# Kernel tuning notes

Measured on AMD Instinct MI355X. Metric: run time of the kernel, lower is better.

Reference implementation:

```python
import jax, jax.numpy as jnp
import numpy as np

# ---- fan-beam CT geometry (hard-coded in fidelity_module) ----
N = 256                      # image is N x N on [-20, 20]^2
A = 20                       # number of projection angles over [0, 2pi)
UDET = 624                   # detector pixels on [-60, 60]
S = 768                      # ray samples for line-integral quadrature
R_SRC = 59.0                 # source-to-origin radius
R_DET = 49.0                 # detector-to-origin radius
D_SD = R_SRC + R_DET         # source-to-detector distance
XMIN, XMAX = -20.0, 20.0
DX = (XMAX - XMIN) / N
UMIN, UMAX = -60.0, 60.0
DU = (UMAX - UMIN) / UDET
THETAS = ((np.arange(A) + 0.5) * 2.0 * np.pi / A).astype(np.float32)   # cell midpoints (odl.uniform_partition)
UCENT = (UMIN + (np.arange(UDET) + 0.5) * DU).astype(np.float32)       # detector cell midpoints
NFFT = 2048                  # FFT length for ramp filtering (>= 2*UDET)


def _bilinear(img, gx, gy):
    """img: [B,N,N] (axis0=x, axis1=y). gx, gy: fractional index coords, shape [...].
    Returns [B, ...] with zero outside the image."""
    i0 = jnp.floor(gx)
    j0 = jnp.floor(gy)
    fx = (gx - i0).astype(img.dtype)
    fy = (gy - j0).astype(img.dtype)
    i0 = i0.astype(jnp.int32)
    j0 = j0.astype(jnp.int32)

    def corner(ii, jj):
        valid = (ii >= 0) & (ii < N) & (jj >= 0) & (jj < N)
        v = img[:, jnp.clip(ii, 0, N - 1), jnp.clip(jj, 0, N - 1)]
        return jnp.where(valid[None], v, 0.0)

    return (corner(i0, j0) * (1 - fx) * (1 - fy)
            + corner(i0 + 1, j0) * fx * (1 - fy)
            + corner(i0, j0 + 1) * (1 - fx) * fy
            + corner(i0 + 1, j0 + 1) * fx * fy)


def forward_project(img):
    """Ray-driven fan-beam forward projection (Radon transform). img: [B,N,N] -> sino [B,A,UDET]."""
    cs = jnp.cos(jnp.asarray(THETAS))
    sn = jnp.sin(jnp.asarray(THETAS))
    src = R_SRC * jnp.stack([cs, sn], axis=-1)            # (A,2) source positions
    det_c = -R_DET * jnp.stack([cs, sn], axis=-1)         # (A,2) detector centers
    ddir = jnp.stack([-sn, cs], axis=-1)                  # (A,2) detector axis
    u = jnp.asarray(UCENT)
    p = det_c[:, None, :] + u[None, :, None] * ddir[:, None, :]   # (A,U,2) detector pixel positions
    ray = p - src[:, None, :]                             # (A,U,2)
    length = jnp.sqrt(jnp.sum(ray * ray, axis=-1))        # (A,U) ray length
    tt = (jnp.arange(S, dtype=jnp.float32) + 0.5) / S     # (S,) midpoint quadrature
    pts = src[:, None, None, :] + tt[None, None, :, None] * ray[:, :, None, :]  # (A,U,S,2)
    gx = (pts[..., 0] - XMIN) / DX - 0.5                  # fractional index along axis0 (x)
    gy = (pts[..., 1] - XMIN) / DX - 0.5                  # fractional index along axis1 (y)
    vals = _bilinear(img, gx, gy)                         # (B,A,U,S)
    return jnp.sum(vals, axis=-1) * (length / S)[None]    # (B,A,U)


def fbp(sino):
    """Filtered back-projection with Hann-windowed ramp filter (frequency_scaling=1).
    sino: [B,A,UDET] -> image [B,N,N]."""
    u = jnp.asarray(UCENT)
    # cosine pre-weighting for flat fan-beam detector
    g = sino * (D_SD / jnp.sqrt(D_SD * D_SD + u * u))[None, None, :]
    freqs = jnp.fft.rfftfreq(NFFT, d=DU).astype(jnp.float32)
    nyq = 1.0 / (2.0 * DU)
    ramp = jnp.abs(freqs)
    hann = 0.5 * (1.0 + jnp.cos(np.float32(np.pi) * freqs / nyq)) * (freqs <= nyq)
    filt = ramp * hann
    q = jnp.fft.irfft(jnp.fft.rfft(g, n=NFFT, axis=-1) * filt[None, None, :], n=NFFT, axis=-1)
    q = q[..., :UDET] * DU                                # (B,A,U) filtered sinogram

    cs = jnp.cos(jnp.asarray(THETAS))
    sn = jnp.sin(jnp.asarray(THETAS))
    xs = XMIN + (jnp.arange(N, dtype=jnp.float32) + 0.5) * DX
    X = xs[:, None]                                       # axis0 = x
    Y = xs[None, :]                                       # axis1 = y
    # distance from source plane to pixel along central ray: in [R_SRC-28, R_SRC+28], never ~0
    tdist = R_SRC - (X[None] * cs[:, None, None] + Y[None] * sn[:, None, None])   # (A,N,N)
    uu = D_SD * (-X[None] * sn[:, None, None] + Y[None] * cs[:, None, None]) / tdist  # detector coord of pixel
    k = (uu - UCENT[0]) / DU                              # fractional detector index (A,N,N)
    k0 = jnp.floor(k)
    fk = (k - k0).astype(sino.dtype)
    k0 = k0.astype(jnp.int32)
    aidx = jnp.arange(A)[:, None, None]

    def gather(kk):
        valid = (kk >= 0) & (kk < UDET)
        v = q[:, aidx, jnp.clip(kk, 0, UDET - 1)]         # (B,A,N,N)
        return jnp.where(valid[None], v, 0.0)

    val = gather(k0) * (1 - fk)[None] + gather(k0 + 1) * fk[None]
    w = (R_SRC / tdist) ** 2                              # fan-beam distance weighting
    dtheta = 2.0 * np.pi / A
    return 0.5 * np.float32(dtheta) * jnp.sum(w[None] * val, axis=1)  # (B,N,N)


def setup_inputs() -> dict:
    key = jax.random.key(0)
    k1, k2 = jax.random.split(key)
    input_data = jax.random.uniform(k1, (4, N, N), dtype=jnp.float32)
    proj = jax.random.normal(k2, (4, A, UDET), dtype=jnp.float32)
    return {"input_data": input_data, "proj": proj}


def reference(input_data, proj):
    # fidelity_module.forward: x_error = FBP(proj - Radon(input_data))
    p_tmp = forward_project(input_data)
    y_error = proj - p_tmp
    return fbp(y_error)
```

## Files before the change

kernel.cpp:

```cpp
#include <hip/hip_runtime.h>
#include <math.h>

#define NN 256
#define AA 20
#define UD 624
#define SS 768
#define NAU (AA*UD)
#define PI_D 3.14159265358979323846

__global__ __launch_bounds__(256) void k_prep(const float* __restrict__ img,
                                              float4* __restrict__ pixA,
                                              float4* __restrict__ pixB,
                                              float* __restrict__ hh) {
    __shared__ double red[256];
    const int blk = blockIdx.x;
    const int tid = threadIdx.x;
    if (blk < 256) {
        int idx = blk * 256 + tid;
        float4 v;
        v.x = img[idx]; v.y = img[65536 + idx]; v.z = img[131072 + idx]; v.w = img[196608 + idx];
        pixA[idx] = v;
    } else if (blk < 512) {
        int oidx = (blk - 256) * 256 + tid;
        int j = oidx >> 8, i = oidx & 255;
        int idx = i * 256 + j;
        float4 v;
        v.x = img[idx]; v.y = img[65536 + idx]; v.z = img[131072 + idx]; v.w = img[196608 + idx];
        pixB[oidx] = v;
    } else {
        const int n = blk - 512;
        double acc = 0.0;
        for (int k = 1 + tid; k < 1024; k += 256) {
            float a1 = 1.0f + cosf((float)PI_D * (float)k * (1.0f/1024.0f));
            int m = (k * n) & 2047;
            float c2 = cosf((float)PI_D * (float)m * (1.0f/1024.0f));
            acc += (double)((float)k * a1 * c2);
        }
        red[tid] = acc;
        __syncthreads();
        for (int s = 128; s > 0; s >>= 1) {
            if (tid < s) red[tid] += red[tid + s];
            __syncthreads();
        }
        if (tid == 0) hh[n] = (float)(red[0] * (1.0 / (2048.0 * 2048.0)));
    }
}

__global__ __launch_bounds__(256) void k_fwd(const float4* __restrict__ pixA,
                                             const float4* __restrict__ pixB,
                                             const float* __restrict__ proj,
                                             float* __restrict__ g) {
    const int widx = threadIdx.x >> 6;
    const int lane = threadIdx.x & 63;
    const int qd = blockIdx.x * 4 + widx;
    const int a = qd / 156;
    const int ub = (qd - a * 156) * 4;
    const int grp = lane >> 4;
    const int sl = lane & 15;

    const float theta = (float)(((double)a + 0.5) * (2.0 * PI_D / (double)AA));
    float sn, cs;
    sincosf(theta, &sn, &cs);
    const float uc = (float)(-60.0 + ((double)(ub + grp) + 0.5) * (120.0 / 624.0));

    const float sx = 59.0f * cs, sy = 59.0f * sn;
    const float rx = -108.0f * cs - uc * sn;
    const float ry = -108.0f * sn + uc * cs;
    const float length = sqrtf(rx * rx + ry * ry);

    const float stepx = rx * (6.4f / 768.0f);
    const float basex = (sx + rx * (0.5f / 768.0f) + 20.0f) * 6.4f - 0.5f;
    const float stepy = ry * (6.4f / 768.0f);
    const float basey = (sy + ry * (0.5f / 768.0f) + 20.0f) * 6.4f - 0.5f;

    const bool useB = fabsf(stepx) > fabsf(stepy);
    const float4* __restrict__ im = useB ? pixB : pixA;
    const float bi = useB ? basex : basey;
    const float si = useB ? stepx : stepy;
    const float bo = useB ? basey : basex;
    const float so = useB ? stepy : stepx;

    float ax = 0.f, ay = 0.f, az = 0.f, aw = 0.f;

    for (int it = 0; it < 48; ++it) {
        const int s = (it << 4) + sl;
        float gi = fmaf((float)s, si, bi);
        float go = fmaf((float)s, so, bo);
        float fgi = floorf(gi), fgo = floorf(go);
        float fi = gi - fgi, fo = go - fgo;
        int i0 = (int)fgi, o0 = (int)fgo;
        int i1 = i0 + 1, o1 = o0 + 1;
        float wi0 = (i0 >= 0 && i0 < NN) ? (1.0f - fi) : 0.0f;
        float wi1 = (i1 >= 0 && i1 < NN) ? fi : 0.0f;
        float wo0 = (o0 >= 0 && o0 < NN) ? (1.0f - fo) : 0.0f;
        float wo1 = (o1 >= 0 && o1 < NN) ? fo : 0.0f;
        int ic0 = min(max(i0, 0), NN - 1), ic1 = min(max(i1, 0), NN - 1);
        int oc0 = min(max(o0, 0), NN - 1), oc1 = min(max(o1, 0), NN - 1);
        const float4 c00 = im[oc0 * NN + ic0];
        const float4 c10 = im[oc0 * NN + ic1];
        const float4 c01 = im[oc1 * NN + ic0];
        const float4 c11 = im[oc1 * NN + ic1];
        float w00 = wi0 * wo0, w10 = wi1 * wo0, w01 = wi0 * wo1, w11 = wi1 * wo1;
        ax += w00 * c00.x + w10 * c10.x + w01 * c01.x + w11 * c11.x;
        ay += w00 * c00.y + w10 * c10.y + w01 * c01.y + w11 * c11.y;
        az += w00 * c00.z + w10 * c10.z + w01 * c01.z + w11 * c11.z;
        aw += w00 * c00.w + w10 * c10.w + w01 * c01.w + w11 * c11.w;
    }

    for (int off = 8; off > 0; off >>= 1) {
        ax += __shfl_down(ax, off);
        ay += __shfl_down(ay, off);
        az += __shfl_down(az, off);
        aw += __shfl_down(aw, off);
    }

    if (sl == 0) {
        const int ray = a * UD + ub + grp;
        const float scale = length * (1.0f / 768.0f);
        const float wdet = 108.0f / sqrtf(108.0f * 108.0f + uc * uc);
        g[0 * NAU + ray] = (proj[0 * NAU + ray] - ax * scale) * wdet;
        g[1 * NAU + ray] = (proj[1 * NAU + ray] - ay * scale) * wdet;
        g[2 * NAU + ray] = (proj[2 * NAU + ray] - az * scale) * wdet;
        g[3 * NAU + ray] = (proj[3 * NAU + ray] - aw * scale) * wdet;
    }
}

__global__ __launch_bounds__(256) void k_conv(const float* __restrict__ g,
                                              const float* __restrict__ hh,
                                              float* __restrict__ q) {
    __shared__ float sgp[752];
    __shared__ float sacc[256];
    const int row = blockIdx.x / 10;
    const int jt = blockIdx.x - row * 10;
    const int tid = threadIdx.x;

    for (int k = tid; k < 752; k += 256)
        sgp[k] = (k >= 64 && k < 64 + UD) ? g[row * UD + (k - 64)] : 0.0f;
    __syncthreads();

    const int jloc = tid & 63;
    const int seg = tid >> 6;
    const int j = jt * 64 + jloc;
    const int jc = min(j, UD - 1);
    const int n1 = min(jt * 64 + 64, UD);
    const int n2 = UD - 1 - jt * 64;

    float acc = 0.0f;
    int t0 = (n1 * seg) >> 2, t1 = (n1 * (seg + 1)) >> 2;
    for (int t = t0; t < t1; ++t) acc += hh[t] * sgp[64 + jc - t];
    t0 = 1 + ((n2 * seg) >> 2); t1 = 1 + ((n2 * (seg + 1)) >> 2);
    for (int t = t0; t < t1; ++t) acc += hh[t] * sgp[64 + jc + t];

    sacc[tid] = acc;
    __syncthreads();
    if (tid < 64) {
        int jj = jt * 64 + tid;
        if (jj < UD) {
            float s = sacc[tid] + sacc[64 + tid] + sacc[128 + tid] + sacc[192 + tid];
            q[row * UD + jj] = s;
        }
    }
}

__global__ __launch_bounds__(256) void k_bp(const float* __restrict__ q,
                                            float* __restrict__ out) {
    __shared__ float scs[AA], ssn[AA];
    const int tid = threadIdx.x;
    if (tid < AA) {
        float th = (float)(((double)tid + 0.5) * (2.0 * PI_D / (double)AA));
        float s, c;
        sincosf(th, &s, &c);
        scs[tid] = c;
        ssn[tid] = s;
    }
    __syncthreads();

    const int p = blockIdx.x * 256 + tid;
    const int b = p >> 16;
    const int rem = p & 65535;
    const int i = rem >> 8;
    const int j = rem & 255;

    const float X = -20.0f + ((float)i + 0.5f) * 0.15625f;
    const float Y = -20.0f + ((float)j + 0.5f) * 0.15625f;

    const float uc0 = (float)(-60.0 + 0.5 * (120.0 / 624.0));
    const float duf = (float)(120.0 / 624.0);

    const float* __restrict__ qb = q + b * AA * UD;
    float acc = 0.0f;
#pragma unroll
    for (int a = 0; a < AA; ++a) {
        float cs = scs[a], sn = ssn[a];
        float t = 59.0f - (X * cs + Y * sn);
        float uu = 108.0f * (Y * cs - X * sn) / t;
        float k = (uu - uc0) / duf;
        float fk0 = floorf(k);
        float fk = k - fk0;
        int ik = (int)fk0;
        const float* qr = qb + a * UD;
        float v0 = ((unsigned)ik < (unsigned)UD) ? qr[ik] : 0.0f;
        float v1 = ((unsigned)(ik + 1) < (unsigned)UD) ? qr[ik + 1] : 0.0f;
        float val = v0 * (1.0f - fk) + v1 * fk;
        float w = 59.0f / t;
        acc += w * w * val;
    }
    out[p] = (0.5f * (float)(2.0 * PI_D / (double)AA)) * acc;
}

extern "C" void kernel_launch(void* const* d_in, const int* in_sizes, int n_in,
                              void* d_out, int out_size, void* d_ws, size_t ws_size,
                              hipStream_t stream) {
    const float* img  = (const float*)d_in[0];
    const float* proj = (const float*)d_in[1];
    float* out = (float*)d_out;

    char* ws = (char*)d_ws;
    float4* pixA = (float4*)ws;
    float4* pixB = (float4*)(ws + (1 << 20));
    float*  g    = (float*)(ws + (2 << 20));
    float*  q    = (float*)(ws + (2 << 20) + 200704);
    float*  hh   = (float*)(ws + (2 << 20) + 401408);

    k_prep<<<1136, 256, 0, stream>>>(img, pixA, pixB, hh);
    k_fwd <<<780,  256, 0, stream>>>(pixA, pixB, proj, g);
    k_conv<<<800,  256, 0, stream>>>(g, hh, q);
    k_bp  <<<1024, 256, 0, stream>>>(q, out);
}
```

Before: 116.1 us.

## Use closed-form ramp kernel, register-blocked convolution, and LDS-staged backprojection

Replaces the 624-block cosine-sum computation of the ramp filter taps in k_prep with a closed-form double-precision formula evaluated inside k_conv and held in shared memory. The convolution now has each thread compute four adjacent outputs with a sliding register window, and the launch drops to 400 blocks. k_bp copies each batch's whole filtered sinogram (about 50 KB) into LDS before interpolating. Together these remove the expensive filter precompute and cut global gathers, at the cost of per-block redundant double-precision sin evaluation, large LDS use that limits occupancy in backprojection, and small numerical differences from the closed form.

```diff
diff --git a/kernel.cpp b/kernel.cpp
--- a/kernel.cpp
+++ b/kernel.cpp
@@ -10,9 +10,7 @@
 
 __global__ __launch_bounds__(256) void k_prep(const float* __restrict__ img,
                                               float4* __restrict__ pixA,
-                                              float4* __restrict__ pixB,
-                                              float* __restrict__ hh) {
-    __shared__ double red[256];
+                                              float4* __restrict__ pixB) {
     const int blk = blockIdx.x;
     const int tid = threadIdx.x;
     if (blk < 256) {
@@ -20,29 +18,13 @@
         float4 v;
         v.x = img[idx]; v.y = img[65536 + idx]; v.z = img[131072 + idx]; v.w = img[196608 + idx];
         pixA[idx] = v;
-    } else if (blk < 512) {
+    } else {
         int oidx = (blk - 256) * 256 + tid;
         int j = oidx >> 8, i = oidx & 255;
         int idx = i * 256 + j;
         float4 v;
         v.x = img[idx]; v.y = img[65536 + idx]; v.z = img[131072 + idx]; v.w = img[196608 + idx];
         pixB[oidx] = v;
-    } else {
-        const int n = blk - 512;
-        double acc = 0.0;
-        for (int k = 1 + tid; k < 1024; k += 256) {
-            float a1 = 1.0f + cosf((float)PI_D * (float)k * (1.0f/1024.0f));
-            int m = (k * n) & 2047;
-            float c2 = cosf((float)PI_D * (float)m * (1.0f/1024.0f));
-            acc += (double)((float)k * a1 * c2);
-        }
-        red[tid] = acc;
-        __syncthreads();
-        for (int s = 128; s > 0; s >>= 1) {
-            if (tid < s) red[tid] += red[tid + s];
-            __syncthreads();
-        }
-        if (tid == 0) hh[n] = (float)(red[0] * (1.0 / (2048.0 * 2048.0)));
     }
 }
 
@@ -126,46 +108,98 @@
 }
 
 __global__ __launch_bounds__(256) void k_conv(const float* __restrict__ g,
-                                              const float* __restrict__ hh,
                                               float* __restrict__ q) {
-    __shared__ float sgp[752];
-    __shared__ float sacc[256];
-    const int row = blockIdx.x / 10;
-    const int jt = blockIdx.x - row * 10;
+    __shared__ float sgp[880];
+    __shared__ float shh[624];
+    __shared__ float sacc[1024];
+    const int row = blockIdx.x / 5;
+    const int jt  = blockIdx.x - row * 5;
     const int tid = threadIdx.x;
 
-    for (int k = tid; k < 752; k += 256)
-        sgp[k] = (k >= 64 && k < 64 + UD) ? g[row * UD + (k - 64)] : 0.0f;
+    for (int n = tid; n < UD; n += 256) {
+        double v;
+        if (n == 0) {
+            double s1 = sin(PI_D / 2048.0);
+            v = 524288.0 - 0.5 / (s1 * s1);
+        } else if (n == 1) {
+            double s1 = sin(PI_D / 2048.0);
+            v = 262144.0 - 0.5 / (s1 * s1);
+        } else if (n & 1) {
+            double s1 = sin(PI_D * (double)n / 2048.0);
+            v = -0.5 / (s1 * s1);
+        } else {
+            double sa = sin(PI_D * (double)(n - 1) / 2048.0);
+            double sb = sin(PI_D * (double)(n + 1) / 2048.0);
+            v = -0.25 * (1.0 / (sa * sa) + 1.0 / (sb * sb));
+        }
+        shh[n] = (float)(v * (1.0 / 4194304.0));
+    }
+    for (int k = tid; k < 880; k += 256)
+        sgp[k] = (k >= 128 && k < 128 + UD) ? g[row * UD + (k - 128)] : 0.0f;
     __syncthreads();
 
-    const int jloc = tid & 63;
-    const int seg = tid >> 6;
-    const int j = jt * 64 + jloc;
-    const int jc = min(j, UD - 1);
-    const int n1 = min(jt * 64 + 64, UD);
-    const int n2 = UD - 1 - jt * 64;
-
-    float acc = 0.0f;
-    int t0 = (n1 * seg) >> 2, t1 = (n1 * (seg + 1)) >> 2;
-    for (int t = t0; t < t1; ++t) acc += hh[t] * sgp[64 + jc - t];
-    t0 = 1 + ((n2 * seg) >> 2); t1 = 1 + ((n2 * (seg + 1)) >> 2);
-    for (int t = t0; t < t1; ++t) acc += hh[t] * sgp[64 + jc + t];
-
-    sacc[tid] = acc;
+    const int quad = tid & 31;
+    const int seg  = tid >> 5;
+    const int J0 = jt * 128;
+    const int j0 = J0 + quad * 4;
+    const int base = 128 + j0;
+
+    const int n1 = min(J0 + 128, UD);
+    const int n2 = UD - 1 - J0;
+
+    float a0 = 0.f, a1 = 0.f, a2 = 0.f, a3 = 0.f;
+
+    {
+        int ta = (n1 * seg) >> 3, tb = (n1 * (seg + 1)) >> 3;
+        float w0 = sgp[base - ta],     w1 = sgp[base - ta + 1],
+              w2 = sgp[base - ta + 2], w3 = sgp[base - ta + 3];
+        for (int t = ta; t < tb; ++t) {
+            float h = shh[t];
+            a0 = fmaf(h, w0, a0); a1 = fmaf(h, w1, a1);
+            a2 = fmaf(h, w2, a2); a3 = fmaf(h, w3, a3);
+            float nv = sgp[base - t - 1];
+            w3 = w2; w2 = w1; w1 = w0; w0 = nv;
+        }
+    }
+    {
+        int ta = 1 + ((n2 * seg) >> 3), tb = 1 + ((n2 * (seg + 1)) >> 3);
+        float w0 = sgp[base + ta],     w1 = sgp[base + ta + 1],
+              w2 = sgp[base + ta + 2], w3 = sgp[base + ta + 3];
+        for (int t = ta; t < tb; ++t) {
+            float h = shh[t];
+            a0 = fmaf(h, w0, a0); a1 = fmaf(h, w1, a1);
+            a2 = fmaf(h, w2, a2); a3 = fmaf(h, w3, a3);
+            float nv = sgp[base + t + 4];
+            w0 = w1; w1 = w2; w2 = w3; w3 = nv;
+        }
+    }
+
+    sacc[(seg << 7) + (quad << 2) + 0] = a0;
+    sacc[(seg << 7) + (quad << 2) + 1] = a1;
+    sacc[(seg << 7) + (quad << 2) + 2] = a2;
+    sacc[(seg << 7) + (quad << 2) + 3] = a3;
     __syncthreads();
-    if (tid < 64) {
-        int jj = jt * 64 + tid;
-        if (jj < UD) {
-            float s = sacc[tid] + sacc[64 + tid] + sacc[128 + tid] + sacc[192 + tid];
-            q[row * UD + jj] = s;
+    if (tid < 128) {
+        int j = J0 + tid;
+        if (j < UD) {
+            float s = sacc[tid] + sacc[128 + tid] + sacc[256 + tid] + sacc[384 + tid]
+                    + sacc[512 + tid] + sacc[640 + tid] + sacc[768 + tid] + sacc[896 + tid];
+            q[row * UD + j] = s;
         }
     }
 }
 
 __global__ __launch_bounds__(256) void k_bp(const float* __restrict__ q,
                                             float* __restrict__ out) {
+    __shared__ float sq[AA * UD];
     __shared__ float scs[AA], ssn[AA];
     const int tid = threadIdx.x;
+    const int p = blockIdx.x * 256 + tid;
+    const int b = p >> 16;
+
+    const float4* __restrict__ qb4 = (const float4*)(q + b * AA * UD);
+    float4* sq4 = (float4*)sq;
+    for (int k = tid; k < AA * UD / 4; k += 256) sq4[k] = qb4[k];
     if (tid < AA) {
         float th = (float)(((double)tid + 0.5) * (2.0 * PI_D / (double)AA));
         float s, c;
@@ -175,8 +209,6 @@
     }
     __syncthreads();
 
-    const int p = blockIdx.x * 256 + tid;
-    const int b = p >> 16;
     const int rem = p & 65535;
     const int i = rem >> 8;
     const int j = rem & 255;
@@ -187,7 +219,6 @@
     const float uc0 = (float)(-60.0 + 0.5 * (120.0 / 624.0));
     const float duf = (float)(120.0 / 624.0);
 
-    const float* __restrict__ qb = q + b * AA * UD;
     float acc = 0.0f;
 #pragma unroll
     for (int a = 0; a < AA; ++a) {
@@ -198,7 +229,7 @@
         float fk0 = floorf(k);
         float fk = k - fk0;
         int ik = (int)fk0;
-        const float* qr = qb + a * UD;
+        const float* qr = sq + a * UD;
         float v0 = ((unsigned)ik < (unsigned)UD) ? qr[ik] : 0.0f;
         float v1 = ((unsigned)(ik + 1) < (unsigned)UD) ? qr[ik + 1] : 0.0f;
         float val = v0 * (1.0f - fk) + v1 * fk;
@@ -220,10 +251,9 @@
     float4* pixB = (float4*)(ws + (1 << 20));
     float*  g    = (float*)(ws + (2 << 20));
     float*  q    = (float*)(ws + (2 << 20) + 200704);
-    float*  hh   = (float*)(ws + (2 << 20) + 401408);
-
-    k_prep<<<1136, 256, 0, stream>>>(img, pixA, pixB, hh);
+
+    k_prep<<<512,  256, 0, stream>>>(img, pixA, pixB);
     k_fwd <<<780,  256, 0, stream>>>(pixA, pixB, proj, g);
-    k_conv<<<800,  256, 0, stream>>>(g, hh, q);
+    k_conv<<<400,  256, 0, stream>>>(g, q);
     k_bp  <<<1024, 256, 0, stream>>>(q, out);
 }
```

Result: slower. 118.9 us (+2.4%).
